# Performance work log

Measured on AMD Instinct MI355X. Metric: run time of the kernel, lower is better.

## Reference

```python
import jax, jax.numpy as jnp
import numpy as np

B, N, C = 4, 1024, 768
H = 12
D = C // H
SCALE = D ** -0.5


def setup_inputs() -> dict:
    key = jax.random.key(0)
    k1, k2, k3, k4, k5 = jax.random.split(key, 5)
    inp = {
        'input': jax.random.normal(k1, (B, N, C), dtype=jnp.float32),
        'input_jvp': jax.random.normal(k2, (B, N, C), dtype=jnp.float32),
        # qkv linear (no bias), proj linear (with bias), torch Linear layout [out, in]
        'W_qkv': jax.random.normal(k3, (3 * C, C), dtype=jnp.float32) * (C ** -0.5),
        'W_proj': jax.random.normal(k4, (C, C), dtype=jnp.float32) * (C ** -0.5),
        'b_proj': jax.random.normal(k5, (C,), dtype=jnp.float32) * 0.02,
    }
    return inp


def _split_heads(t):
    t = t.reshape(B, N, 3, H, D).transpose(2, 0, 3, 1, 4)
    return t[0], t[1], t[2]


def reference(input, input_jvp, W_qkv, W_proj, b_proj):
    # LinearLinear: primal gets full affine, tangent gets linear part only
    qkv = jnp.einsum('bnc,oc->bno', input, W_qkv)
    qkv_jvp = jnp.einsum('bnc,oc->bno', input_jvp, W_qkv)
    q, k, v = _split_heads(qkv)
    q_jvp, k_jvp, v_jvp = _split_heads(qkv_jvp)

    q = q * SCALE
    attn = jax.nn.softmax(jnp.einsum('bhnd,bhmd->bhnm', q, k), axis=-1)
    x = jnp.einsum('bhnm,bhmd->bhnd', attn, v)

    q_jvp = q_jvp * SCALE
    A_jvp = jnp.einsum('bhnd,bhmd->bhnm', q_jvp, k)
    B_jvp = jnp.einsum('bhnd,bhmd->bhnm', q, k_jvp)
    C_jvp = jnp.einsum('bhnm,bhmd->bhnd', attn, v_jvp)
    dm_by_dr = A_jvp + B_jvp
    # softmax JVP: attn * (dm - rowsum(dm * attn))
    attn_filter_1 = dm_by_dr * attn
    row = jnp.sum(dm_by_dr * attn, axis=-1, keepdims=True)  # = diag(dm @ attn^T)
    attn_filter = attn_filter_1 - row * attn
    x_jvp = jnp.einsum('bhnm,bhmd->bhnd', attn_filter, v) + C_jvp

    x = x.transpose(0, 2, 1, 3).reshape(B, N, C)
    x_jvp = x_jvp.transpose(0, 2, 1, 3).reshape(B, N, C)

    x = jnp.einsum('bnc,oc->bno', x, W_proj) + b_proj
    x_jvp = jnp.einsum('bnc,oc->bno', x_jvp, W_proj)
    return (x, x_jvp)
```

## Files before the change

kernel.cpp:

```cpp
#include <hip/hip_runtime.h>

constexpr int Bn = 4;
constexpr int Nn = 1024;
constexpr int Cn = 768;
constexpr int Hn = 12;
constexpr int Dn = 64;
constexpr float SCALE_Q = 0.125f;
constexpr int SEG = Bn * Nn * Cn;
constexpr int HND = Hn * Nn * Dn;
constexpr int NDn = Nn * Dn;

typedef __attribute__((ext_vector_type(8))) short bf16x8;
typedef __attribute__((ext_vector_type(4))) float f32x4;

__device__ __forceinline__ unsigned short f2bf(float f) {
    union { float f; unsigned u; } v; v.f = f;
    unsigned r = v.u + 0x7fffu + ((v.u >> 16) & 1u);
    return (unsigned short)(r >> 16);
}
__device__ __forceinline__ float bf2f(unsigned short b) {
    union { unsigned u; float f; } v; v.u = ((unsigned)b) << 16;
    return v.f;
}
__device__ __forceinline__ bf16x8 ldfrag(const unsigned short* base, int boff) {
    return *(const bf16x8*)((const char*)base + boff);
}
#define MFMA(a, b, c) __builtin_amdgcn_mfma_f32_16x16x32_bf16((a), (b), (c), 0, 0, 0)


__global__ __launch_bounds__(256)
void conv_k(const float* __restrict__ a0, const float* __restrict__ a1,
            unsigned short* __restrict__ dst)
{
    const int P = SEG / 4;
    const int j = blockIdx.x * 256 + threadIdx.x;
    const int arr = j / P;
    const int i = (j - arr * P) * 4;
    const float* __restrict__ src = arr ? a1 : a0;
    const float4 f = *(const float4*)(src + i);
    const float ff[4] = {f.x, f.y, f.z, f.w};
    ushort4 h, lo;
#pragma unroll
    for (int t = 0; t < 4; ++t) {
        const unsigned short hv = f2bf(ff[t]);
        (&h.x)[t] = hv;
        (&lo.x)[t] = f2bf(ff[t] - bf2f(hv));
    }
    *(ushort4*)(dst + (size_t)(2 * arr) * SEG + i) = h;
    *(ushort4*)(dst + (size_t)(2 * arr + 1) * SEG + i) = lo;
}

template<int MODE>
__global__ __launch_bounds__(256, 2)
void gemm_mfma(const unsigned short* __restrict__ Abase,
               const float* __restrict__ W, const float* __restrict__ bias,
               unsigned short* __restrict__ qkv, float* __restrict__ out)
{
    __shared__ unsigned short sAh[128 * 64];
    __shared__ unsigned short sAl[128 * 64];
    __shared__ unsigned short sBh[128 * 64];
    __shared__ unsigned short sBl[128 * 64];

    const int tid = threadIdx.x;
    const int z = blockIdx.z;
    const int row0 = blockIdx.y << 7;
    const int col0 = blockIdx.x << 7;
    const int l = tid & 63, w = tid >> 6;
    const int wr = w >> 1, wc = w & 1;
    const int h4 = l >> 4, l15 = l & 15;
    const int sw = (l15 & 7) << 4;

    const unsigned short* __restrict__ Ah = Abase + (size_t)(2 * z) * SEG;
    const unsigned short* __restrict__ Al = Abase + (size_t)(2 * z + 1) * SEG;

    f32x4 acc[4][4];
#pragma unroll
    for (int m = 0; m < 4; ++m)
#pragma unroll
        for (int n = 0; n < 4; ++n)
            acc[m][n] = (f32x4){0.f, 0.f, 0.f, 0.f};

    for (int k0 = 0; k0 < Cn; k0 += 64) {
        __syncthreads();
#pragma unroll
        for (int it = 0; it < 4; ++it) {
            const int idx = it * 256 + tid;
            const int row = idx >> 3, s = idx & 7;
            const size_t go = (size_t)(row0 + row) * Cn + k0 + 8 * s;
            const int boff = row * 128 + ((s ^ (row & 7)) << 4);
            *(bf16x8*)((char*)sAh + boff) = *(const bf16x8*)(Ah + go);
            *(bf16x8*)((char*)sAl + boff) = *(const bf16x8*)(Al + go);
        }
#pragma unroll
        for (int it = 0; it < 8; ++it) {
            const int idx = it * 256 + tid;
            const int row = idx >> 4, s4 = idx & 15;
            const float4 f = *(const float4*)(W + (size_t)(col0 + row) * Cn + k0 + 4 * s4);
            const float ff[4] = {f.x, f.y, f.z, f.w};
            ushort4 h, lo;
#pragma unroll
            for (int t = 0; t < 4; ++t) {
                const unsigned short hv = f2bf(ff[t]);
                (&h.x)[t] = hv;
                (&lo.x)[t] = f2bf(ff[t] - bf2f(hv));
            }
            const int boff = row * 128 + (((s4 >> 1) ^ (row & 7)) << 4) + ((s4 & 1) << 3);
            *(ushort4*)((char*)sBh + boff) = h;
            *(ushort4*)((char*)sBl + boff) = lo;
        }
        __syncthreads();
#pragma unroll
        for (int c = 0; c < 2; ++c) {
            bf16x8 ah[4], al[4], bh[4], bl[4];
#pragma unroll
            for (int m = 0; m < 4; ++m) {
                const int boff = (64 * wr + 16 * m + l15) * 128 + ((((c << 2) | h4) << 4) ^ sw);
                ah[m] = ldfrag(sAh, boff);
                al[m] = ldfrag(sAl, boff);
            }
#pragma unroll
            for (int n = 0; n < 4; ++n) {
                const int boff = (64 * wc + 16 * n + l15) * 128 + ((((c << 2) | h4) << 4) ^ sw);
                bh[n] = ldfrag(sBh, boff);
                bl[n] = ldfrag(sBl, boff);
            }
#pragma unroll
            for (int m = 0; m < 4; ++m)
#pragma unroll
                for (int n = 0; n < 4; ++n) {
                    acc[m][n] = MFMA(ah[m], bh[n], acc[m][n]);
                    acc[m][n] = MFMA(ah[m], bl[n], acc[m][n]);
                    acc[m][n] = MFMA(al[m], bh[n], acc[m][n]);
                }
        }
    }

    if (MODE == 0) {
#pragma unroll
        for (int n = 0; n < 4; ++n) {
            const int colb = col0 + 64 * wc + 16 * n;
            const int t = colb / Cn;
            const int rem = colb - t * Cn;
            const int hh = rem >> 6;
            const int d = (rem & 63) + l15;
            const float sc = (t == 0) ? SCALE_Q : 1.0f;
            const int t2 = t + 3 * z;
            unsigned short* __restrict__ dh = qkv + (size_t)(2 * t2) * SEG;
            unsigned short* __restrict__ dl = dh + SEG;
#pragma unroll
            for (int m = 0; m < 4; ++m)
#pragma unroll
                for (int r = 0; r < 4; ++r) {
                    const int row = row0 + 64 * wr + 16 * m + 4 * h4 + r;
                    const int b = row >> 10, nq = row & 1023;
                    const size_t ad = (size_t)(b * Hn + hh) * NDn + nq * 64 + d;
                    const float vv = acc[m][n][r] * sc;
                    const unsigned short hv = f2bf(vv);
                    dh[ad] = hv;
                    dl[ad] = f2bf(vv - bf2f(hv));
                }
        }
    } else {
#pragma unroll
        for (int n = 0; n < 4; ++n) {
            const int col = col0 + 64 * wc + 16 * n + l15;
            const float bi = (z == 0) ? bias[col] : 0.0f;
#pragma unroll
            for (int m = 0; m < 4; ++m)
#pragma unroll
                for (int r = 0; r < 4; ++r) {
                    const int row = row0 + 64 * wr + 16 * m + 4 * h4 + r;
                    out[(size_t)z * SEG + (size_t)row * Cn + col] = acc[m][n][r] + bi;
                }
        }
    }
}

__global__ __launch_bounds__(256, 2)
void attn_mfma(unsigned short* __restrict__ wsu)
{
    __shared__ unsigned short sKV[4][64 * 64];
    __shared__ unsigned short sP[4][4][16 * 64];

    const int tid = threadIdx.x;
    const int l = tid & 63;
    const int w = tid >> 6;
    const int h4 = l >> 4;
    const int l15 = l & 15;
    const int sw = (l15 & 7) << 4;

    const int bh = blockIdx.x;
    const int r0 = blockIdx.y << 6;

    const unsigned short* __restrict__ Bq = wsu + 4 * (size_t)SEG + (size_t)bh * NDn;
    const unsigned short* __restrict__ qh = Bq;
    const unsigned short* __restrict__ kh = Bq + 2 * (size_t)SEG;
    const unsigned short* __restrict__ vh = Bq + 4 * (size_t)SEG;
    const unsigned short* __restrict__ qjh = Bq + 6 * (size_t)SEG;
    const unsigned short* __restrict__ kjh = Bq + 8 * (size_t)SEG;
    const unsigned short* __restrict__ vjh = Bq + 10 * (size_t)SEG;

    bf16x8 qhi[2], qlo[2], qjhi[2], qjlo[2];
    {
        const int qrow = r0 + w * 16 + l15;
#pragma unroll
        for (int c = 0; c < 2; ++c) {
            const size_t o = (size_t)qrow * 64 + c * 32 + h4 * 8;
            qhi[c] = *(const bf16x8*)(qh + o);
            qlo[c] = *(const bf16x8*)(qh + SEG + o);
            qjhi[c] = *(const bf16x8*)(qjh + o);
            qjlo[c] = *(const bf16x8*)(qjh + SEG + o);
        }
    }

    f32x4 mold = {-3.0e38f, -3.0e38f, -3.0e38f, -3.0e38f};
    f32x4 l_run = {0.f, 0.f, 0.f, 0.f};
    f32x4 ar_run = {0.f, 0.f, 0.f, 0.f};
    f32x4 ax[4], ac[4], ad[4];
#pragma unroll
    for (int ds = 0; ds < 4; ++ds) {
        ax[ds] = (f32x4){0.f, 0.f, 0.f, 0.f};
        ac[ds] = (f32x4){0.f, 0.f, 0.f, 0.f};
        ad[ds] = (f32x4){0.f, 0.f, 0.f, 0.f};
    }

    for (int jt = 0; jt < Nn; jt += 64) {
        __syncthreads();
#pragma unroll
        for (int it = 0; it < 2; ++it) {
            const int idx = it * 256 + tid;
            const int row = idx >> 3, s = idx & 7;
            const size_t go = (size_t)(jt + row) * 64 + 8 * s;
            const int boff = row * 128 + ((s ^ (row & 7)) << 4);
            *(bf16x8*)((char*)sKV[0] + boff) = *(const bf16x8*)(kh + go);
            *(bf16x8*)((char*)sKV[1] + boff) = *(const bf16x8*)(kh + SEG + go);
            *(bf16x8*)((char*)sKV[2] + boff) = *(const bf16x8*)(kjh + go);
            *(bf16x8*)((char*)sKV[3] + boff) = *(const bf16x8*)(kjh + SEG + go);
        }
        __syncthreads();

        f32x4 S[4], DM[4];
#pragma unroll
        for (int kt = 0; kt < 4; ++kt) {
            f32x4 s = {0.f, 0.f, 0.f, 0.f};
            f32x4 dm = {0.f, 0.f, 0.f, 0.f};
#pragma unroll
            for (int c = 0; c < 2; ++c) {
                const int boff = (l15 + (kt << 4)) * 128 + (((h4 << 4) | (c << 6)) ^ sw);
                const bf16x8 khi = ldfrag(sKV[0], boff);
                const bf16x8 klo = ldfrag(sKV[1], boff);
                const bf16x8 jhi = ldfrag(sKV[2], boff);
                const bf16x8 jlo = ldfrag(sKV[3], boff);
                s = MFMA(qhi[c], khi, s);
                s = MFMA(qhi[c], klo, s);
                s = MFMA(qlo[c], khi, s);
                dm = MFMA(qjhi[c], khi, dm);
                dm = MFMA(qjhi[c], klo, dm);
                dm = MFMA(qjlo[c], khi, dm);
                dm = MFMA(qhi[c], jhi, dm);
                dm = MFMA(qhi[c], jlo, dm);
                dm = MFMA(qlo[c], jhi, dm);
            }
            S[kt] = s; DM[kt] = dm;
        }

        f32x4 tmax, mnew, alpha;
#pragma unroll
        for (int r = 0; r < 4; ++r)
            tmax[r] = fmaxf(fmaxf(S[0][r], S[1][r]), fmaxf(S[2][r], S[3][r]));
#pragma unroll
        for (int m = 1; m < 16; m <<= 1)
#pragma unroll
            for (int r = 0; r < 4; ++r)
                tmax[r] = fmaxf(tmax[r], __shfl_xor(tmax[r], m));
#pragma unroll
        for (int r = 0; r < 4; ++r) {
            mnew[r] = fmaxf(mold[r], tmax[r]);
            alpha[r] = __expf(mold[r] - mnew[r]);
            mold[r] = mnew[r];
        }
        f32x4 lsum = {0.f, 0.f, 0.f, 0.f};
        f32x4 arsum = {0.f, 0.f, 0.f, 0.f};
#pragma unroll
        for (int kt = 0; kt < 4; ++kt) {
            const int key = (kt << 4) + l15;
#pragma unroll
            for (int r = 0; r < 4; ++r) {
                const float p = __expf(S[kt][r] - mnew[r]);
                const float pd = p * DM[kt][r];
                lsum[r] += p;
                arsum[r] += pd;
                const int qq = (h4 << 2) + r;
                const int boff = qq * 128 +
                    (((key & 7) << 1) | ((((key >> 3) ^ (qq & 7)) << 4)));
                const unsigned short ph = f2bf(p);
                const unsigned short pdh = f2bf(pd);
                *(unsigned short*)((char*)sP[w][0] + boff) = ph;
                *(unsigned short*)((char*)sP[w][1] + boff) = f2bf(p - bf2f(ph));
                *(unsigned short*)((char*)sP[w][2] + boff) = pdh;
                *(unsigned short*)((char*)sP[w][3] + boff) = f2bf(pd - bf2f(pdh));
            }
        }
#pragma unroll
        for (int r = 0; r < 4; ++r) {
            l_run[r] = l_run[r] * alpha[r] + lsum[r];
            ar_run[r] = ar_run[r] * alpha[r] + arsum[r];
        }
#pragma unroll
        for (int ds = 0; ds < 4; ++ds) {
            ax[ds] *= alpha; ac[ds] *= alpha; ad[ds] *= alpha;
        }

        __syncthreads();
        {
            const int j = tid & 63, dgrp = tid >> 6;
#pragma unroll
            for (int dd = 0; dd < 4; ++dd) {
                const int d0 = dgrp * 16 + dd * 4;
                const size_t go = (size_t)(jt + j) * 64 + d0;
                const ushort4 a = *(const ushort4*)(vh + go);
                const ushort4 b = *(const ushort4*)(vh + SEG + go);
                const ushort4 c = *(const ushort4*)(vjh + go);
                const ushort4 e = *(const ushort4*)(vjh + SEG + go);
#pragma unroll
                for (int i = 0; i < 4; ++i) {
                    const int d = d0 + i;
                    const int boff = d * 128 +
                        (((j & 7) << 1) | ((((j >> 3) ^ (d & 7)) << 4)));
                    *(unsigned short*)((char*)sKV[0] + boff) = (&a.x)[i];
                    *(unsigned short*)((char*)sKV[1] + boff) = (&b.x)[i];
                    *(unsigned short*)((char*)sKV[2] + boff) = (&c.x)[i];
                    *(unsigned short*)((char*)sKV[3] + boff) = (&e.x)[i];
                }
            }
        }
        __syncthreads();

#pragma unroll
        for (int kc = 0; kc < 2; ++kc) {
            const int pxo = ((h4 << 4) | (kc << 6)) ^ sw;
            const bf16x8 phi = ldfrag(sP[w][0], l15 * 128 + pxo);
            const bf16x8 plo = ldfrag(sP[w][1], l15 * 128 + pxo);
            const bf16x8 dhi = ldfrag(sP[w][2], l15 * 128 + pxo);
            const bf16x8 dlo = ldfrag(sP[w][3], l15 * 128 + pxo);
#pragma unroll
            for (int ds = 0; ds < 4; ++ds) {
                const int boff = (l15 + (ds << 4)) * 128 + pxo;
                const bf16x8 vhi = ldfrag(sKV[0], boff);
                const bf16x8 vlo = ldfrag(sKV[1], boff);
                const bf16x8 wjh = ldfrag(sKV[2], boff);
                const bf16x8 wjl = ldfrag(sKV[3], boff);
                ax[ds] = MFMA(phi, vhi, ax[ds]);
                ax[ds] = MFMA(phi, vlo, ax[ds]);
                ax[ds] = MFMA(plo, vhi, ax[ds]);
                ac[ds] = MFMA(phi, wjh, ac[ds]);
                ac[ds] = MFMA(phi, wjl, ac[ds]);
                ac[ds] = MFMA(plo, wjh, ac[ds]);
                ad[ds] = MFMA(dhi, vhi, ad[ds]);
                ad[ds] = MFMA(dhi, vlo, ad[ds]);
                ad[ds] = MFMA(dlo, vhi, ad[ds]);
            }
        }
    }

#pragma unroll
    for (int m = 1; m < 16; m <<= 1)
#pragma unroll
        for (int r = 0; r < 4; ++r) {
            l_run[r] += __shfl_xor(l_run[r], m);
            ar_run[r] += __shfl_xor(ar_run[r], m);
        }
    const int b = bh / Hn;
    const int hh = bh - b * Hn;
    unsigned short* __restrict__ xh = wsu;
    unsigned short* __restrict__ xl = wsu + (size_t)SEG;
    unsigned short* __restrict__ xjh = wsu + 2 * (size_t)SEG;
    unsigned short* __restrict__ xjl = wsu + 3 * (size_t)SEG;
#pragma unroll
    for (int r = 0; r < 4; ++r) {
        const int qg = r0 + w * 16 + (h4 << 2) + r;
        const float invl = 1.0f / l_run[r];
        const float rowv = ar_run[r] * invl;
        const size_t base = ((size_t)(b * Nn + qg)) * Cn + hh * Dn + l15;
#pragma unroll
        for (int ds = 0; ds < 4; ++ds) {
            const float x = ax[ds][r] * invl;
            const float xjv = fmaf(-rowv, x, (ad[ds][r] + ac[ds][r]) * invl);
            const size_t ad2 = base + ds * 16;
            const unsigned short h0 = f2bf(x);
            xh[ad2] = h0;
            xl[ad2] = f2bf(x - bf2f(h0));
            const unsigned short h1 = f2bf(xjv);
            xjh[ad2] = h1;
            xjl[ad2] = f2bf(xjv - bf2f(h1));
        }
    }
}

extern "C" void kernel_launch(void* const* d_in, const int* in_sizes, int n_in,
                              void* d_out, int out_size, void* d_ws, size_t ws_size,
                              hipStream_t stream)
{
    const float* input  = (const float*)d_in[0];
    const float* inputj = (const float*)d_in[1];
    const float* W_qkv  = (const float*)d_in[2];
    const float* W_proj = (const float*)d_in[3];
    const float* b_proj = (const float*)d_in[4];
    float* out = (float*)d_out;
    unsigned short* wsu = (unsigned short*)d_ws;
    unsigned short* regA = wsu;
    unsigned short* regB = wsu + 4 * (size_t)SEG;

    conv_k<<<2 * (SEG / 4) / 256, 256, 0, stream>>>(input, inputj, regA);
    gemm_mfma<0><<<dim3(18, 32, 2), 256, 0, stream>>>(regA, W_qkv, nullptr,
                                                      regB, nullptr);
    attn_mfma<<<dim3(48, 16), 256, 0, stream>>>(wsu);
    gemm_mfma<1><<<dim3(6, 32, 2), 256, 0, stream>>>(regA, W_proj, b_proj,
                                                     nullptr, out);
}
```

Before: 400.9 us.

## Pre-split weights, register-prefetch GEMM/attention tiles, transpose V in QKV epilogue

Weights are now split into bf16 hi/lo once by a separate conversion kernel, instead of being re-split inside every GEMM tile load. The output buffer and the spare workspace serve as scratch for these copies. The GEMM and attention loops prefetch the next K/V tiles into registers while the current tile is computed, and raise wave priority around the MFMA sections. The QKV epilogue now writes V (and V-tangent) transposed, so attention can stage V with vector loads rather than scattered 2-byte shared stores. Costs are two extra small kernel launches, higher register pressure from the prefetch buffers, and strided scalar writes for V in the epilogue.

```diff
diff --git a/kernel.cpp b/kernel.cpp
--- a/kernel.cpp
+++ b/kernel.cpp
@@ -7,8 +7,9 @@
 constexpr int Dn = 64;
 constexpr float SCALE_Q = 0.125f;
 constexpr int SEG = Bn * Nn * Cn;
-constexpr int HND = Hn * Nn * Dn;
 constexpr int NDn = Nn * Dn;
+constexpr int WQ_ELE = 3 * Cn * Cn;
+constexpr int WP_ELE = Cn * Cn;
 
 typedef __attribute__((ext_vector_type(8))) short bf16x8;
 typedef __attribute__((ext_vector_type(4))) float f32x4;
@@ -50,10 +51,30 @@
     *(ushort4*)(dst + (size_t)(2 * arr + 1) * SEG + i) = lo;
 }
 
+__global__ __launch_bounds__(256)
+void conv_w(const float* __restrict__ src, unsigned short* __restrict__ dh,
+            unsigned short* __restrict__ dl)
+{
+    const int i = (blockIdx.x * 256 + threadIdx.x) * 4;
+    const float4 f = *(const float4*)(src + i);
+    const float ff[4] = {f.x, f.y, f.z, f.w};
+    ushort4 h, lo;
+#pragma unroll
+    for (int t = 0; t < 4; ++t) {
+        const unsigned short hv = f2bf(ff[t]);
+        (&h.x)[t] = hv;
+        (&lo.x)[t] = f2bf(ff[t] - bf2f(hv));
+    }
+    *(ushort4*)(dh + i) = h;
+    *(ushort4*)(dl + i) = lo;
+}
+
 template<int MODE>
 __global__ __launch_bounds__(256, 2)
 void gemm_mfma(const unsigned short* __restrict__ Abase,
-               const float* __restrict__ W, const float* __restrict__ bias,
+               const unsigned short* __restrict__ Wh,
+               const unsigned short* __restrict__ Wl,
+               const float* __restrict__ bias,
                unsigned short* __restrict__ qkv, float* __restrict__ out)
 {
     __shared__ unsigned short sAh[128 * 64];
@@ -69,6 +90,8 @@
     const int wr = w >> 1, wc = w & 1;
     const int h4 = l >> 4, l15 = l & 15;
     const int sw = (l15 & 7) << 4;
+    const int srow = tid >> 3;
+    const int ss = tid & 7;
 
     const unsigned short* __restrict__ Ah = Abase + (size_t)(2 * z) * SEG;
     const unsigned short* __restrict__ Al = Abase + (size_t)(2 * z + 1) * SEG;
@@ -80,34 +103,35 @@
         for (int n = 0; n < 4; ++n)
             acc[m][n] = (f32x4){0.f, 0.f, 0.f, 0.f};
 
+    bf16x8 pAh[4], pAl[4], pBh[4], pBl[4];
+
+#define G_LOADT(K0_) {                                                        \
+    _Pragma("unroll")                                                         \
+    for (int it = 0; it < 4; ++it) {                                          \
+        const int row = srow + 32 * it;                                       \
+        const size_t goA = (size_t)(row0 + row) * Cn + (K0_) + 8 * ss;        \
+        const size_t goB = (size_t)(col0 + row) * Cn + (K0_) + 8 * ss;        \
+        pAh[it] = *(const bf16x8*)(Ah + goA);                                 \
+        pAl[it] = *(const bf16x8*)(Al + goA);                                 \
+        pBh[it] = *(const bf16x8*)(Wh + goB);                                 \
+        pBl[it] = *(const bf16x8*)(Wl + goB);                                 \
+    } }
+
+    G_LOADT(0);
+
     for (int k0 = 0; k0 < Cn; k0 += 64) {
         __syncthreads();
 #pragma unroll
         for (int it = 0; it < 4; ++it) {
-            const int idx = it * 256 + tid;
-            const int row = idx >> 3, s = idx & 7;
-            const size_t go = (size_t)(row0 + row) * Cn + k0 + 8 * s;
-            const int boff = row * 128 + ((s ^ (row & 7)) << 4);
-            *(bf16x8*)((char*)sAh + boff) = *(const bf16x8*)(Ah + go);
-            *(bf16x8*)((char*)sAl + boff) = *(const bf16x8*)(Al + go);
-        }
-#pragma unroll
-        for (int it = 0; it < 8; ++it) {
-            const int idx = it * 256 + tid;
-            const int row = idx >> 4, s4 = idx & 15;
-            const float4 f = *(const float4*)(W + (size_t)(col0 + row) * Cn + k0 + 4 * s4);
-            const float ff[4] = {f.x, f.y, f.z, f.w};
-            ushort4 h, lo;
-#pragma unroll
-            for (int t = 0; t < 4; ++t) {
-                const unsigned short hv = f2bf(ff[t]);
-                (&h.x)[t] = hv;
-                (&lo.x)[t] = f2bf(ff[t] - bf2f(hv));
-            }
-            const int boff = row * 128 + (((s4 >> 1) ^ (row & 7)) << 4) + ((s4 & 1) << 3);
-            *(ushort4*)((char*)sBh + boff) = h;
-            *(ushort4*)((char*)sBl + boff) = lo;
-        }
+            const int row = srow + 32 * it;
+            const int boff = row * 128 + ((ss ^ (row & 7)) << 4);
+            *(bf16x8*)((char*)sAh + boff) = pAh[it];
+            *(bf16x8*)((char*)sAl + boff) = pAl[it];
+            *(bf16x8*)((char*)sBh + boff) = pBh[it];
+            *(bf16x8*)((char*)sBl + boff) = pBl[it];
+        }
+        const int kn = (k0 + 64 < Cn) ? k0 + 64 : 0;
+        G_LOADT(kn);
         __syncthreads();
 #pragma unroll
         for (int c = 0; c < 2; ++c) {
@@ -153,7 +177,9 @@
                 for (int r = 0; r < 4; ++r) {
                     const int row = row0 + 64 * wr + 16 * m + 4 * h4 + r;
                     const int b = row >> 10, nq = row & 1023;
-                    const size_t ad = (size_t)(b * Hn + hh) * NDn + nq * 64 + d;
+                    const size_t ad = (size_t)(b * Hn + hh) * NDn +
+                        (t == 2 ? (size_t)d * Nn + nq
+                                : (size_t)nq * 64 + d);
                     const float vv = acc[m][n][r] * sc;
                     const unsigned short hv = f2bf(vv);
                     dh[ad] = hv;
@@ -188,17 +214,20 @@
     const int h4 = l >> 4;
     const int l15 = l & 15;
     const int sw = (l15 & 7) << 4;
+    const int rA = tid >> 3;
+    const int ss = tid & 7;
+    const int rB = rA + 32;
 
     const int bh = blockIdx.x;
     const int r0 = blockIdx.y << 6;
 
     const unsigned short* __restrict__ Bq = wsu + 4 * (size_t)SEG + (size_t)bh * NDn;
-    const unsigned short* __restrict__ qh = Bq;
-    const unsigned short* __restrict__ kh = Bq + 2 * (size_t)SEG;
-    const unsigned short* __restrict__ vh = Bq + 4 * (size_t)SEG;
-    const unsigned short* __restrict__ qjh = Bq + 6 * (size_t)SEG;
-    const unsigned short* __restrict__ kjh = Bq + 8 * (size_t)SEG;
-    const unsigned short* __restrict__ vjh = Bq + 10 * (size_t)SEG;
+    const unsigned short* __restrict__ qh   = Bq;
+    const unsigned short* __restrict__ kh   = Bq + 2 * (size_t)SEG;
+    const unsigned short* __restrict__ vth  = Bq + 4 * (size_t)SEG;
+    const unsigned short* __restrict__ qjh  = Bq + 6 * (size_t)SEG;
+    const unsigned short* __restrict__ kjh  = Bq + 8 * (size_t)SEG;
+    const unsigned short* __restrict__ vjth = Bq + 10 * (size_t)SEG;
 
     bf16x8 qhi[2], qlo[2], qjhi[2], qjlo[2];
     {
@@ -224,22 +253,41 @@
         ad[ds] = (f32x4){0.f, 0.f, 0.f, 0.f};
     }
 
+    bf16x8 kr0[4], kr1[4], vr0[4], vr1[4];
+    const int ba = rA * 128 + ((ss ^ (rA & 7)) << 4);
+    const int bb = rB * 128 + ((ss ^ (rA & 7)) << 4);
+
+#define A_LOADK(JT_) {                                                         \
+    const size_t ga = (size_t)((JT_) + rA) * 64 + 8 * ss;                      \
+    const size_t gb = (size_t)((JT_) + rB) * 64 + 8 * ss;                      \
+    kr0[0] = *(const bf16x8*)(kh + ga);        kr1[0] = *(const bf16x8*)(kh + gb); \
+    kr0[1] = *(const bf16x8*)(kh + SEG + ga);  kr1[1] = *(const bf16x8*)(kh + SEG + gb); \
+    kr0[2] = *(const bf16x8*)(kjh + ga);       kr1[2] = *(const bf16x8*)(kjh + gb); \
+    kr0[3] = *(const bf16x8*)(kjh + SEG + ga); kr1[3] = *(const bf16x8*)(kjh + SEG + gb); }
+
+#define A_LOADV(JT_) {                                                         \
+    const size_t ga = (size_t)rA * Nn + (JT_) + 8 * ss;                        \
+    const size_t gb = (size_t)rB * Nn + (JT_) + 8 * ss;                        \
+    vr0[0] = *(const bf16x8*)(vth + ga);        vr1[0] = *(const bf16x8*)(vth + gb); \
+    vr0[1] = *(const bf16x8*)(vth + SEG + ga);  vr1[1] = *(const bf16x8*)(vth + SEG + gb); \
+    vr0[2] = *(const bf16x8*)(vjth + ga);       vr1[2] = *(const bf16x8*)(vjth + gb); \
+    vr0[3] = *(const bf16x8*)(vjth + SEG + ga); vr1[3] = *(const bf16x8*)(vjth + SEG + gb); }
+
+#define A_WRITE(R0_, R1_) {                                                    \
+    *(bf16x8*)((char*)sKV[0] + ba) = R0_[0]; *(bf16x8*)((char*)sKV[0] + bb) = R1_[0]; \
+    *(bf16x8*)((char*)sKV[1] + ba) = R0_[1]; *(bf16x8*)((char*)sKV[1] + bb) = R1_[1]; \
+    *(bf16x8*)((char*)sKV[2] + ba) = R0_[2]; *(bf16x8*)((char*)sKV[2] + bb) = R1_[2]; \
+    *(bf16x8*)((char*)sKV[3] + ba) = R0_[3]; *(bf16x8*)((char*)sKV[3] + bb) = R1_[3]; }
+
+    A_LOADK(0);
+
     for (int jt = 0; jt < Nn; jt += 64) {
         __syncthreads();
-#pragma unroll
-        for (int it = 0; it < 2; ++it) {
-            const int idx = it * 256 + tid;
-            const int row = idx >> 3, s = idx & 7;
-            const size_t go = (size_t)(jt + row) * 64 + 8 * s;
-            const int boff = row * 128 + ((s ^ (row & 7)) << 4);
-            *(bf16x8*)((char*)sKV[0] + boff) = *(const bf16x8*)(kh + go);
-            *(bf16x8*)((char*)sKV[1] + boff) = *(const bf16x8*)(kh + SEG + go);
-            *(bf16x8*)((char*)sKV[2] + boff) = *(const bf16x8*)(kjh + go);
-            *(bf16x8*)((char*)sKV[3] + boff) = *(const bf16x8*)(kjh + SEG + go);
-        }
+        A_WRITE(kr0, kr1);
         __syncthreads();
 
         f32x4 S[4], DM[4];
+        __builtin_amdgcn_s_setprio(1);
 #pragma unroll
         for (int kt = 0; kt < 4; ++kt) {
             f32x4 s = {0.f, 0.f, 0.f, 0.f};
@@ -263,6 +311,10 @@
             }
             S[kt] = s; DM[kt] = dm;
         }
+        __builtin_amdgcn_s_setprio(0);
+
+        A_LOADV(jt);
+        A_LOADK((jt + 64) & (Nn - 1));
 
         f32x4 tmax, mnew, alpha;
 #pragma unroll
@@ -312,30 +364,10 @@
         }
 
         __syncthreads();
-        {
-            const int j = tid & 63, dgrp = tid >> 6;
-#pragma unroll
-            for (int dd = 0; dd < 4; ++dd) {
-                const int d0 = dgrp * 16 + dd * 4;
-                const size_t go = (size_t)(jt + j) * 64 + d0;
-                const ushort4 a = *(const ushort4*)(vh + go);
-                const ushort4 b = *(const ushort4*)(vh + SEG + go);
-                const ushort4 c = *(const ushort4*)(vjh + go);
-                const ushort4 e = *(const ushort4*)(vjh + SEG + go);
-#pragma unroll
-                for (int i = 0; i < 4; ++i) {
-                    const int d = d0 + i;
-                    const int boff = d * 128 +
-                        (((j & 7) << 1) | ((((j >> 3) ^ (d & 7)) << 4)));
-                    *(unsigned short*)((char*)sKV[0] + boff) = (&a.x)[i];
-                    *(unsigned short*)((char*)sKV[1] + boff) = (&b.x)[i];
-                    *(unsigned short*)((char*)sKV[2] + boff) = (&c.x)[i];
-                    *(unsigned short*)((char*)sKV[3] + boff) = (&e.x)[i];
-                }
-            }
-        }
-        __syncthreads();
-
+        A_WRITE(vr0, vr1);
+        __syncthreads();
+
+        __builtin_amdgcn_s_setprio(1);
 #pragma unroll
         for (int kc = 0; kc < 2; ++kc) {
             const int pxo = ((h4 << 4) | (kc << 6)) ^ sw;
@@ -361,6 +393,7 @@
                 ad[ds] = MFMA(dlo, vhi, ad[ds]);
             }
         }
+        __builtin_amdgcn_s_setprio(0);
     }
 
 #pragma unroll
@@ -410,11 +443,17 @@
     unsigned short* wsu = (unsigned short*)d_ws;
     unsigned short* regA = wsu;
     unsigned short* regB = wsu + 4 * (size_t)SEG;
+    unsigned short* wqh = (unsigned short*)d_out;
+    unsigned short* wql = wqh + (size_t)WQ_ELE;
+    unsigned short* wph = regB;
+    unsigned short* wpl = wph + (size_t)WP_ELE;
 
     conv_k<<<2 * (SEG / 4) / 256, 256, 0, stream>>>(input, inputj, regA);
-    gemm_mfma<0><<<dim3(18, 32, 2), 256, 0, stream>>>(regA, W_qkv, nullptr,
+    conv_w<<<(WQ_ELE / 4) / 256, 256, 0, stream>>>(W_qkv, wqh, wql);
+    gemm_mfma<0><<<dim3(18, 32, 2), 256, 0, stream>>>(regA, wqh, wql, nullptr,
                                                       regB, nullptr);
     attn_mfma<<<dim3(48, 16), 256, 0, stream>>>(wsu);
-    gemm_mfma<1><<<dim3(6, 32, 2), 256, 0, stream>>>(regA, W_proj, b_proj,
+    conv_w<<<(WP_ELE / 4) / 256, 256, 0, stream>>>(W_proj, wph, wpl);
+    gemm_mfma<1><<<dim3(6, 32, 2), 256, 0, stream>>>(regA, wph, wpl, b_proj,
                                                      nullptr, out);
 }
```

Result: no change. 398.5 us (-0.6%).
